# Kernel optimization log

Hardware: AMD Instinct MI355X
Metric: run time of the kernel (lower is better)

Reference implementation:

```python
import jax, jax.numpy as jnp
import numpy as np

THRESH = 0.5
IOU_THR = 0.3
TOP_K = 512

# standard YOLOv3 anchors for strides 32/16/8 (grids 13/26/52)
ANCHORS_13 = jnp.array([[116., 90.], [156., 198.], [373., 326.]], dtype=jnp.float32)
ANCHORS_26 = jnp.array([[30., 61.], [62., 45.], [59., 119.]], dtype=jnp.float32)
ANCHORS_52 = jnp.array([[10., 13.], [16., 30.], [33., 23.]], dtype=jnp.float32)


def _decode(out, stride, anchors):
    # out: [B, 3*(5+C), H, W] -> [B, H, W, 3, 5+C] (matches permute(0,2,3,1).reshape)
    B, _, H, W = out.shape
    o = jnp.transpose(out, (0, 2, 3, 1)).reshape(B, H, W, 3, -1)
    conf = jax.nn.sigmoid(o[..., 4])          # [B,H,W,3]
    xy = jax.nn.sigmoid(o[..., 0:2])          # sigmoid on x,y as in _filter
    gy = jnp.arange(H, dtype=o.dtype)[None, :, None, None]   # idxs[:,1]
    gx = jnp.arange(W, dtype=o.dtype)[None, None, :, None]   # idxs[:,2]
    cy = (gy + xy[..., 1]) * stride
    cx = (gx + xy[..., 0]) * stride
    w = anchors[:, 0] * jnp.exp(o[..., 2])    # anchors broadcast over anchor dim
    h = anchors[:, 1] * jnp.exp(o[..., 3])
    cls = jnp.argmax(o[..., 5:], axis=-1).astype(o.dtype)
    n = jnp.broadcast_to(jnp.arange(B, dtype=o.dtype)[:, None, None, None], conf.shape)
    w0, h0 = w * 0.5, h * 0.5
    boxes = jnp.stack([conf, cx - w0, cy - h0, cx + w0, cy + h0, cls, n], axis=-1)
    return boxes.reshape(-1, 7), conf.reshape(-1)


def _iou_matrix(b):
    # b: [K,4] = x1,y1,x2,y2 -> [K,K] IoU
    area = jnp.clip(b[:, 2] - b[:, 0], 0) * jnp.clip(b[:, 3] - b[:, 1], 0)
    xx1 = jnp.maximum(b[:, None, 0], b[None, :, 0])
    yy1 = jnp.maximum(b[:, None, 1], b[None, :, 1])
    xx2 = jnp.minimum(b[:, None, 2], b[None, :, 2])
    yy2 = jnp.minimum(b[:, None, 3], b[None, :, 3])
    inter = jnp.clip(xx2 - xx1, 0) * jnp.clip(yy2 - yy1, 0)
    return inter / (area[:, None] + area[None, :] - inter + 1e-9)


def _detect(output_13, output_26, output_52):
    b13, c13 = _decode(output_13, 32.0, ANCHORS_13)
    b26, c26 = _decode(output_26, 16.0, ANCHORS_26)
    b52, c52 = _decode(output_52, 8.0, ANCHORS_52)
    boxes = jnp.concatenate([b13, b26, b52], axis=0)      # [N,7]
    conf = jnp.concatenate([c13, c26, c52], axis=0)       # [N]
    # threshold filter (mask instead of nonzero-compaction for fixed shapes)
    scores = jnp.where(conf > THRESH, conf, 0.0)
    top_scores, idx = jax.lax.top_k(scores, TOP_K)        # sorted descending
    cand = boxes[idx]                                      # [K,7]
    valid = top_scores > THRESH
    iou = _iou_matrix(cand[:, 1:5])
    ar = jnp.arange(TOP_K)

    def body(i, keep):
        sup = keep[i] & (iou[i] > IOU_THR) & (ar > i)
        return keep & ~sup

    keep = jax.lax.fori_loop(0, TOP_K, body, valid)
    # zero out suppressed / invalid rows; rows: [conf, x1, y1, x2, y2, cls, batch]
    return cand * keep[:, None].astype(cand.dtype)


def setup_inputs() -> dict:
    key = jax.random.key(0)
    k1, k2, k3 = jax.random.split(key, 3)
    return {
        "output_13": jax.random.normal(k1, (32, 255, 13, 13), dtype=jnp.float32),
        "output_26": jax.random.normal(k2, (32, 255, 26, 26), dtype=jnp.float32),
        "output_52": jax.random.normal(k3, (32, 255, 52, 52), dtype=jnp.float32),
    }


def reference(output_13, output_26, output_52):
    return _detect(output_13, output_26, output_52)
```

## Files before the change

kernel.cpp:

```cpp
#include <hip/hip_runtime.h>

#define N13E 16224
#define N26E 64896
#define NTOT 340704
#define BASE26 16224
#define BASE52 81120
#define KMAX 2048
#define TOPK 512

__device__ __forceinline__ float sigm(float x) { return 1.0f / (1.0f + expf(-x)); }

template <int HW>
__device__ __forceinline__ float load_logit(const float* __restrict__ p, int local) {
    int ba = local / HW;
    int hw = local - ba * HW;
    int b = ba / 3;
    int a = ba - b * 3;
    return p[(b * 255 + a * 85 + 4) * HW + hw];
}

__global__ void __launch_bounds__(256) k_hist(const float* __restrict__ p13,
                                              const float* __restrict__ p26,
                                              const float* __restrict__ p52,
                                              unsigned* __restrict__ hist) {
    int t = blockIdx.x * 256 + threadIdx.x;
    if (t >= NTOT) return;
    float logit;
    if (t < N13E)               logit = load_logit<169>(p13, t);
    else if (t < N13E + N26E)   logit = load_logit<676>(p26, t - N13E);
    else                        logit = load_logit<2704>(p52, t - (N13E + N26E));
    float conf = sigm(logit);
    if (conf > 0.5f) {
        unsigned bin = (__float_as_uint(conf) >> 12) - 0x3F000u;
        bin = (bin > 2047u) ? 2047u : bin;
        atomicAdd(&hist[bin], 1u);
    }
}

template <int HW, int W, int BASE>
__device__ __forceinline__ void compact_decode_one(const float* __restrict__ p, int local, unsigned thrv,
                                                   float strideF,
                                                   float aw0, float ah0, float aw1, float ah1,
                                                   float aw2, float ah2,
                                                   unsigned* __restrict__ cnt,
                                                   unsigned long long* __restrict__ keys,
                                                   float* __restrict__ candAll) {
    int ba = local / HW;
    int hw = local - ba * HW;
    int b = ba / 3;
    int a = ba - b * 3;
    float logit = p[(b * 255 + a * 85 + 4) * HW + hw];
    float conf = sigm(logit);
    unsigned bits = __float_as_uint(conf);
    if (conf > 0.5f && bits >= thrv) {
        unsigned pos = atomicAdd(cnt, 1u);
        if (pos < (unsigned)KMAX) {
            unsigned concat = (unsigned)(BASE + (b * HW + hw) * 3 + a);
            keys[pos] = (((unsigned long long)bits) << 32) | (unsigned long long)(0xFFFFFFFFu - concat);
            int h = hw / W;
            int wc = hw - h * W;
            int cb = b * 255 + a * 85;
            const float* cls_base = p + (size_t)(cb + 5) * HW + hw;
            float bestv = cls_base[0];
            int bestc = 0;
#pragma unroll
            for (int c = 1; c < 80; ++c) {
                float v = cls_base[(size_t)c * HW];
                if (v > bestv) { bestv = v; bestc = c; }
            }
            float t0 = p[(size_t)(cb + 0) * HW + hw];
            float t1 = p[(size_t)(cb + 1) * HW + hw];
            float t2 = p[(size_t)(cb + 2) * HW + hw];
            float t3 = p[(size_t)(cb + 3) * HW + hw];
            float aw = (a == 0) ? aw0 : ((a == 1) ? aw1 : aw2);
            float ah = (a == 0) ? ah0 : ((a == 1) ? ah1 : ah2);
            float sx = sigm(t0);
            float sy = sigm(t1);
            float bw = aw * expf(t2);
            float bh = ah * expf(t3);
            float cx = ((float)wc + sx) * strideF;
            float cy = ((float)h + sy) * strideF;
            float w0 = bw * 0.5f, h0 = bh * 0.5f;
            float* row = candAll + pos * 7;
            row[0] = conf;
            row[1] = cx - w0;
            row[2] = cy - h0;
            row[3] = cx + w0;
            row[4] = cy + h0;
            row[5] = (float)bestc;
            row[6] = (float)b;
        }
    }
}

__global__ void __launch_bounds__(512) k_compact_scan_decode(const float* __restrict__ p13,
                                                             const float* __restrict__ p26,
                                                             const float* __restrict__ p52,
                                                             const unsigned* __restrict__ hist,
                                                             unsigned* __restrict__ cnt,
                                                             unsigned long long* __restrict__ keys,
                                                             float* __restrict__ candAll) {
    __shared__ unsigned tot[512];
    __shared__ unsigned thrS;
    int tid = threadIdx.x;

    unsigned loc[4]; unsigned s = 0u;
#pragma unroll
    for (int k = 0; k < 4; ++k) { loc[k] = hist[2047 - (tid * 4 + k)]; s += loc[k]; }
    tot[tid] = s;
    __syncthreads();
    for (int off = 1; off < 512; off <<= 1) {
        unsigned u = (tid >= off) ? tot[tid - off] : 0u;
        __syncthreads();
        tot[tid] += u;
        __syncthreads();
    }
    unsigned excl = tot[tid] - s;
    unsigned total = tot[511];
    if (total < (unsigned)TOPK) {
        if (tid == 0) thrS = 0x3F000001u;
    } else {
        unsigned run = excl;
#pragma unroll
        for (int k = 0; k < 4; ++k) {
            unsigned c = run + loc[k];
            if (run < (unsigned)TOPK && c >= (unsigned)TOPK) {
                int bin = 2047 - (tid * 4 + k);
                thrS = ((unsigned)(bin + 0x3F000)) << 12;
            }
            run = c;
        }
    }
    __syncthreads();
    unsigned thrv = thrS;

    int t = blockIdx.x * 512 + tid;
    if (t >= NTOT) return;
    if (t < N13E)
        compact_decode_one<169, 13, 0>(p13, t, thrv, 32.0f,
                                       116.f, 90.f, 156.f, 198.f, 373.f, 326.f, cnt, keys, candAll);
    else if (t < N13E + N26E)
        compact_decode_one<676, 26, BASE26>(p26, t - N13E, thrv, 16.0f,
                                            30.f, 61.f, 62.f, 45.f, 59.f, 119.f, cnt, keys, candAll);
    else
        compact_decode_one<2704, 52, BASE52>(p52, t - (N13E + N26E), thrv, 8.0f,
                                             10.f, 13.f, 16.f, 30.f, 33.f, 23.f, cnt, keys, candAll);
}

__global__ void __launch_bounds__(512) k_rank_gather_mask(const unsigned* __restrict__ cnt,
                                                          const unsigned long long* __restrict__ keys,
                                                          const float* __restrict__ candAll,
                                                          float* __restrict__ candSorted,
                                                          unsigned long long* __restrict__ smaskG) {
    __shared__ unsigned long long keysL[KMAX];
    __shared__ unsigned long long sortedL[TOPK];
    __shared__ unsigned short sortedIdxL[TOPK];
    __shared__ float candL[TOPK * 7];
    int tid = threadIdx.x;

    unsigned n = *cnt; if (n > (unsigned)KMAX) n = (unsigned)KMAX;
    int npad = ((int)n + 7) & ~7;
    for (int j = tid; j < npad; j += 512) keysL[j] = (j < (int)n) ? keys[j] : 0ull;
    sortedL[tid] = 0ull;
    __syncthreads();
    unsigned long long mine[4]; unsigned rk[4]; int nown = 0;
#pragma unroll
    for (int k = 0; k < 4; ++k) {
        int idx = tid + k * 512;
        if (idx < (int)n) { mine[nown] = keysL[idx]; rk[nown] = 0u; ++nown; }
    }
    for (int j = 0; j < npad; j += 8) {
        unsigned long long kk[8];
#pragma unroll
        for (int u = 0; u < 8; ++u) kk[u] = keysL[j + u];
        for (int m = 0; m < nown; ++m) {
            unsigned acc = 0u;
#pragma unroll
            for (int u = 0; u < 8; ++u) acc += (kk[u] > mine[m]) ? 1u : 0u;
            rk[m] += acc;
        }
    }
    for (int m = 0; m < nown; ++m) {
        unsigned r = rk[m];
        if (r < (unsigned)TOPK) {
            sortedL[r] = mine[m];
            sortedIdxL[r] = (unsigned short)(tid + m * 512);
        }
    }
    __syncthreads();

    {
        unsigned long long key = sortedL[tid];
        float* row = candL + tid * 7;
        if ((unsigned)(key >> 32) == 0u) {
#pragma unroll
            for (int q = 0; q < 7; ++q) row[q] = 0.0f;
        } else {
            const float* src = candAll + (int)sortedIdxL[tid] * 7;
#pragma unroll
            for (int q = 0; q < 7; ++q) row[q] = src[q];
        }
    }
    __syncthreads();

    if (blockIdx.x == 0) {
        for (int p = tid; p < TOPK * 7; p += 512) candSorted[p] = candL[p];
    }

    int wv = tid >> 6;
    int lane = tid & 63;
    int gwave = blockIdx.x * 8 + wv;
#pragma unroll
    for (int q = 0; q < 16; ++q) {
        int word = gwave * 16 + q;
        int i = word >> 3, jw = word & 7;
        int j = jw * 64 + lane;
        const float* ri = candL + i * 7;
        const float* rj = candL + j * 7;
        float ix1 = ri[1], iy1 = ri[2], ix2 = ri[3], iy2 = ri[4];
        float ai = fmaxf(ix2 - ix1, 0.f) * fmaxf(iy2 - iy1, 0.f);
        float jx1 = rj[1], jy1 = rj[2], jx2 = rj[3], jy2 = rj[4];
        float aj = fmaxf(jx2 - jx1, 0.f) * fmaxf(jy2 - jy1, 0.f);
        float xx1 = fmaxf(ix1, jx1), yy1 = fmaxf(iy1, jy1);
        float xx2 = fminf(ix2, jx2), yy2 = fminf(iy2, jy2);
        float inter = fmaxf(xx2 - xx1, 0.f) * fmaxf(yy2 - yy1, 0.f);
        float iou = inter / (((ai + aj) - inter) + 1e-9f);
        bool bit = (j > i) && (iou > 0.3f);
        unsigned long long m = __ballot(bit);
        if (lane == 0) smaskG[word] = m;
    }
}

__global__ void __launch_bounds__(512) k_sweep(const float* __restrict__ cand,
                                               const unsigned long long* __restrict__ smaskG,
                                               float* __restrict__ out) {
    __shared__ unsigned long long smask[TOPK * 8];
    __shared__ unsigned long long live[8], keepw[8];
    int tid = threadIdx.x;
    for (int p = tid; p < TOPK * 8; p += 512) smask[p] = smaskG[p];
    bool validt = cand[tid * 7] > 0.5f;
    unsigned long long bal = __ballot(validt);
    if ((tid & 63) == 0) live[tid >> 6] = bal;
    __syncthreads();
    if (tid < 64) {
        int lane = tid;
        int lw = lane & 7;
        unsigned long long r = 0ull;
#pragma unroll
        for (int w = 0; w < 8; ++w) {
            unsigned long long lvw = live[w];
#pragma unroll 8
            for (int b2 = 0; b2 < 64; ++b2) {
                int i = w * 64 + b2;
                unsigned long long rowv = smask[i * 8 + lw];
                unsigned rlo = (unsigned)__builtin_amdgcn_readlane((int)(unsigned)(r & 0xFFFFFFFFull), w);
                unsigned rhi = (unsigned)__builtin_amdgcn_readlane((int)(unsigned)(r >> 32), w);
                unsigned long long rw = (((unsigned long long)rhi) << 32) | (unsigned long long)rlo;
                bool acc = (((lvw >> b2) & 1ull) != 0ull) && (((rw >> b2) & 1ull) == 0ull);
                if (acc) r |= rowv;
            }
        }
        if (lane < 8) keepw[lane] = live[lane] & ~r;
    }
    __syncthreads();
    for (int p = tid; p < TOPK * 7; p += 512) {
        int i = p / 7;
        unsigned long long kb = (keepw[i >> 6] >> (i & 63)) & 1ull;
        out[p] = kb ? cand[p] : 0.0f;
    }
}

extern "C" void kernel_launch(void* const* d_in, const int* in_sizes, int n_in,
                              void* d_out, int out_size, void* d_ws, size_t ws_size,
                              hipStream_t stream) {
    const float* p13 = (const float*)d_in[0];
    const float* p26 = (const float*)d_in[1];
    const float* p52 = (const float*)d_in[2];
    float* out = (float*)d_out;
    char* ws = (char*)d_ws;

    unsigned* hist             = (unsigned*)(ws + 0);
    unsigned* cnt              = (unsigned*)(ws + 8192);
    unsigned long long* keys   = (unsigned long long*)(ws + 8704);
    float* candAll             = (float*)(ws + 25088);
    float* candSorted          = (float*)(ws + 82432);
    unsigned long long* smaskG = (unsigned long long*)(ws + 96768);

    hipMemsetAsync(ws, 0, 8196, stream);

    int gh = (NTOT + 255) / 256;
    int gc = (NTOT + 511) / 512;
    k_hist<<<gh, 256, 0, stream>>>(p13, p26, p52, hist);
    k_compact_scan_decode<<<gc, 512, 0, stream>>>(p13, p26, p52, hist, cnt, keys, candAll);
    k_rank_gather_mask<<<32, 512, 0, stream>>>(cnt, keys, candAll, candSorted, smaskG);
    k_sweep<<<1, 512, 0, stream>>>(candSorted, smaskG, out);
}
```

Baseline: 233.5 us.

## Replace serial greedy NMS sweep with parallel fixed-point iteration

The NMS sweep kernel used to walk all 512 candidates one after another inside a single wavefront, using readlane to carry the suppression state between steps. It now runs a Jacobi-style fixed-point iteration across all 8 wavefronts. In each round every wave ORs the suppression masks of the currently kept boxes for its 64-bit word, reduces the result with xor-shuffles, and updates the keep words until nothing changes. This removes the long serial dependency chain. In exchange the number of rounds depends on how deep the suppression chains are in the data, and each round costs several block-wide barriers.

```diff
diff --git a/kernel.cpp b/kernel.cpp
--- a/kernel.cpp
+++ b/kernel.cpp
@@ -235,37 +235,47 @@
                                                const unsigned long long* __restrict__ smaskG,
                                                float* __restrict__ out) {
     __shared__ unsigned long long smask[TOPK * 8];
-    __shared__ unsigned long long live[8], keepw[8];
+    __shared__ unsigned long long live[8], keepS[8], supS[8];
+    __shared__ int changedS;
     int tid = threadIdx.x;
+    int lane = tid & 63;
+    int wv = tid >> 6;
+
     for (int p = tid; p < TOPK * 8; p += 512) smask[p] = smaskG[p];
     bool validt = cand[tid * 7] > 0.5f;
     unsigned long long bal = __ballot(validt);
-    if ((tid & 63) == 0) live[tid >> 6] = bal;
-    __syncthreads();
-    if (tid < 64) {
-        int lane = tid;
-        int lw = lane & 7;
+    if (lane == 0) { live[wv] = bal; keepS[wv] = bal; }
+    __syncthreads();
+
+    for (;;) {
+        unsigned long long kw[8];
+#pragma unroll
+        for (int k = 0; k < 8; ++k) kw[k] = keepS[k];
         unsigned long long r = 0ull;
 #pragma unroll
-        for (int w = 0; w < 8; ++w) {
-            unsigned long long lvw = live[w];
-#pragma unroll 8
-            for (int b2 = 0; b2 < 64; ++b2) {
-                int i = w * 64 + b2;
-                unsigned long long rowv = smask[i * 8 + lw];
-                unsigned rlo = (unsigned)__builtin_amdgcn_readlane((int)(unsigned)(r & 0xFFFFFFFFull), w);
-                unsigned rhi = (unsigned)__builtin_amdgcn_readlane((int)(unsigned)(r >> 32), w);
-                unsigned long long rw = (((unsigned long long)rhi) << 32) | (unsigned long long)rlo;
-                bool acc = (((lvw >> b2) & 1ull) != 0ull) && (((rw >> b2) & 1ull) == 0ull);
-                if (acc) r |= rowv;
-            }
-        }
-        if (lane < 8) keepw[lane] = live[lane] & ~r;
-    }
-    __syncthreads();
+        for (int k = 0; k < 8; ++k) {
+            int j = lane + (k << 6);
+            unsigned long long m = smask[j * 8 + wv];
+            unsigned long long kbit = (kw[k] >> lane) & 1ull;
+            r |= m & (0ull - kbit);
+        }
+#pragma unroll
+        for (int off = 32; off >= 1; off >>= 1) r |= __shfl_xor(r, off, 64);
+        if (lane == 0) supS[wv] = r;
+        __syncthreads();
+        if (tid == 0) changedS = 0;
+        __syncthreads();
+        if (tid < 8) {
+            unsigned long long nk = live[tid] & ~supS[tid];
+            if (nk != keepS[tid]) { keepS[tid] = nk; changedS = 1; }
+        }
+        __syncthreads();
+        if (!changedS) break;
+    }
+
     for (int p = tid; p < TOPK * 7; p += 512) {
         int i = p / 7;
-        unsigned long long kb = (keepw[i >> 6] >> (i & 63)) & 1ull;
+        unsigned long long kb = (keepS[i >> 6] >> (i & 63)) & 1ull;
         out[p] = kb ? cand[p] : 0.0f;
     }
 }
```

After: 209.0 us. -10.5%, faster.
